# Performance work log

Measured on AMD Instinct MI355X. Metric: run time of the kernel, lower is better.

## Reference

```python
import jax, jax.numpy as jnp
import numpy as np
import math

B, S, D, H, NF = 2, 2048, 1024, 16, 4
DH = D // H


def setup_inputs() -> dict:
    key = jax.random.key(0)
    ks = jax.random.split(key, 8)
    scale = 0.01 / math.sqrt(D)  # rough attenuated-kaiming scale for projections
    return {
        "x": jax.random.normal(ks[0], (B, S, D), dtype=jnp.float32),
        "weights": jax.random.uniform(ks[1], (1, NF), dtype=jnp.float32),
        "Wq": jax.random.normal(ks[2], (D, D), dtype=jnp.float32) * scale,
        "bq": jnp.zeros((D,), dtype=jnp.float32),
        "Wk": jax.random.normal(ks[3], (D, D), dtype=jnp.float32) * scale,
        "bk": jnp.zeros((D,), dtype=jnp.float32),
        "Wv": jax.random.normal(ks[4], (D, D), dtype=jnp.float32) * scale,
        "bv": jnp.zeros((D,), dtype=jnp.float32),
        "Wout": jax.random.normal(ks[5], (NF, D, D), dtype=jnp.float32) / math.sqrt(D),
        "bout": jnp.zeros((NF, D), dtype=jnp.float32),
    }


def reference(x, weights, Wq, bq, Wk, bk, Wv, bv, Wout, bout):
    # projections (torch Linear: x @ W.T + b)
    q = x @ Wq.T + bq  # [B,S,D]
    k = x @ Wk.T + bk
    v = x @ Wv.T + bv
    # split heads -> [B,H,S,DH]
    split = lambda t: t.reshape(B, S, H, DH).transpose(0, 2, 1, 3)
    q, k, v = split(q), split(k), split(v)
    # scores with causal additive mask of -10000 (as in get_attention_mask)
    scores = jnp.einsum("bhqd,bhkd->bhqk", q, k) / math.sqrt(DH)
    i = jnp.arange(S)
    causal = (i[None, :] <= i[:, None])  # [S,S] True where allowed
    mask = (1.0 - causal.astype(scores.dtype)) * -10000.0
    attn = jax.nn.softmax(scores + mask, axis=-1)
    # dropout is disabled (p=0.0)
    out = jnp.einsum("bhqk,bhkd->bhqd", attn, v)  # [B,H,S,DH]
    out = out.transpose(0, 2, 1, 3).reshape(B, S, D)
    # WeightedFunctions: per-function Linear(d,d) combined by weights[0]
    w0 = weights[0]  # [NF]
    Weff = jnp.einsum("f,fod->od", w0, Wout)  # [D,D]
    beff = w0 @ bout  # [D]
    return out @ Weff.T + beff
```

## Files before the change

### kernel.cpp

```cpp
#include <hip/hip_runtime.h>

typedef unsigned short u16;
typedef __bf16 bf16_t;
typedef bf16_t bf16x8 __attribute__((ext_vector_type(8)));
typedef bf16_t bf16x4 __attribute__((ext_vector_type(4)));
typedef float f32x4 __attribute__((ext_vector_type(4)));
typedef u16 u16x8 __attribute__((ext_vector_type(8)));
typedef u16 u16x4 __attribute__((ext_vector_type(4)));

#define DEV __device__ __forceinline__

DEV u16 f2bf(float f) {
  unsigned u = __float_as_uint(f);
  u += 0x7FFFu + ((u >> 16) & 1u);
  return (u16)(u >> 16);
}

DEV void async_ld16(const void* g, void* lds_wave_uniform) {
  __builtin_amdgcn_global_load_lds(
      (const __attribute__((address_space(1))) void*)g,
      (__attribute__((address_space(3))) void*)lds_wave_uniform, 16, 0, 0);
}

DEV int KF(int r) { return (r & 3) ^ ((r >> 2) & 1); }

__global__ __launch_bounds__(256) void prep_kernel(
    const float* __restrict__ x, const float* __restrict__ Wq,
    const float* __restrict__ Wk, const float* __restrict__ Wv,
    const float* __restrict__ w4, const float* __restrict__ Wout,
    const float* __restrict__ bout, u16* __restrict__ xbf,
    u16* __restrict__ wqkv, u16* __restrict__ Weff, float* __restrict__ beff) {
  constexpr int NX = 1048576;
  constexpr int NW = 262144;
  const int stride = gridDim.x * 256;
  for (int id = blockIdx.x * 256 + threadIdx.x; id < NX + 3 * NW + NW;
       id += stride) {
    if (id < NX) {
      const float4 v = ((const float4*)x)[id];
      u16x4 o;
      o[0] = f2bf(v.x); o[1] = f2bf(v.y); o[2] = f2bf(v.z); o[3] = f2bf(v.w);
      ((u16x4*)xbf)[id] = o;
    } else if (id < NX + 3 * NW) {
      const int wi = id - NX;
      const int which = wi >> 18, j = wi & (NW - 1);
      const float* src = which == 0 ? Wq : (which == 1 ? Wk : Wv);
      const float4 v = ((const float4*)src)[j];
      u16x4 o;
      o[0] = f2bf(v.x); o[1] = f2bf(v.y); o[2] = f2bf(v.z); o[3] = f2bf(v.w);
      ((u16x4*)wqkv)[wi] = o;
    } else {
      const int i = id - NX - 3 * NW;
      const float w0 = w4[0], w1 = w4[1], w2 = w4[2], w3 = w4[3];
      const float4* W = (const float4*)Wout;
      const float4 a = W[i], b1 = W[NW + i], b2 = W[2 * NW + i],
                   b3 = W[3 * NW + i];
      u16x4 o;
      o[0] = f2bf(w0 * a.x + w1 * b1.x + w2 * b2.x + w3 * b3.x);
      o[1] = f2bf(w0 * a.y + w1 * b1.y + w2 * b2.y + w3 * b3.y);
      o[2] = f2bf(w0 * a.z + w1 * b1.z + w2 * b2.z + w3 * b3.z);
      o[3] = f2bf(w0 * a.w + w1 * b1.w + w2 * b2.w + w3 * b3.w);
      ((u16x4*)Weff)[i] = o;
      if (i < 256) {
        const float4* B4 = (const float4*)bout;
        const float4 ba = B4[i], c1 = B4[256 + i], c2 = B4[512 + i],
                     c3 = B4[768 + i];
        float4 ob;
        ob.x = w0 * ba.x + w1 * c1.x + w2 * c2.x + w3 * c3.x;
        ob.y = w0 * ba.y + w1 * c1.y + w2 * c2.y + w3 * c3.y;
        ob.z = w0 * ba.z + w1 * c1.z + w2 * c2.z + w3 * c3.z;
        ob.w = w0 * ba.w + w1 * c1.w + w2 * c2.w + w3 * c3.w;
        ((float4*)beff)[i] = ob;
      }
    }
  }
}

#define GEMM_PIPELINE_LOOP(A_, B_, m0_, n0_, K_)                               \
  int rA[2], oA[2], dstc[2];                                                   \
  _Pragma("unroll") for (int j = 0; j < 2; ++j) {                              \
    const int c = (j * 4 + w) * 64 + lane;                                     \
    rA[j] = c >> 2;                                                            \
    oA[j] = ((c & 3) ^ KF(rA[j])) * 8;                                         \
    dstc[j] = (j * 4 + w) * 512;                                               \
  }                                                                            \
  auto stage = [&](int buf, int kt) {                                          \
    _Pragma("unroll") for (int j = 0; j < 2; ++j) {                            \
      async_ld16(A_ + (m0_ + rA[j]) * K_ + kt + oA[j],                         \
                 &LDS[buf * 4096 + dstc[j]]);                                  \
      async_ld16(B_ + (n0_ + rA[j]) * K_ + kt + oA[j],                         \
                 &LDS[12288 + buf * 4096 + dstc[j]]);                          \
    }                                                                          \
  };                                                                           \
  f32x4 acc[4][4] = {};                                                        \
  stage(0, 0);                                                                 \
  stage(1, 32);                                                                \
  const int nt = K_ / 32;                                                      \
  int cur = 0, stg = 2;                                                        \
  for (int t = 0; t < nt; ++t) {                                               \
    if (t == nt - 1)                                                           \
      asm volatile("s_waitcnt vmcnt(0)\ns_barrier" ::: "memory");              \
    else                                                                       \
      asm volatile("s_waitcnt vmcnt(4)\ns_barrier" ::: "memory");              \
    __builtin_amdgcn_sched_barrier(0);                                         \
    if (t + 2 < nt) stage(stg, (t + 2) * 32);                                  \
    bf16x8 af[4], bfr[4];                                                      \
    _Pragma("unroll") for (int i = 0; i < 4; ++i) {                            \
      const int ra = wr * 64 + i * 16 + l15;                                   \
      const int rb = wc * 64 + i * 16 + l15;                                   \
      af[i] = *(const bf16x8*)&LDS[cur * 4096 + ra * 32 + ((l4 ^ KF(ra)) * 8)];\
      bfr[i] = *(const bf16x8*)&LDS[12288 + cur * 4096 + rb * 32 +             \
                                    ((l4 ^ KF(rb)) * 8)];                      \
    }                                                                          \
    __builtin_amdgcn_s_setprio(1);                                             \
    _Pragma("unroll") for (int i = 0; i < 4; ++i)                              \
        _Pragma("unroll") for (int j = 0; j < 4; ++j)                          \
            acc[i][j] = __builtin_amdgcn_mfma_f32_16x16x32_bf16(               \
                af[i], bfr[j], acc[i][j], 0, 0, 0);                            \
    __builtin_amdgcn_s_setprio(0);                                             \
    cur = cur == 2 ? 0 : cur + 1;                                              \
    stg = stg == 2 ? 0 : stg + 1;                                              \
  }

__global__ __launch_bounds__(256) void gemm_bt_kernel(
    const u16* __restrict__ A, const u16* __restrict__ Bw,
    const float* __restrict__ bias, float* __restrict__ C, int M, int N, int K) {
  __shared__ u16 LDS[24576];
  const int tid = threadIdx.x;
  const int w = tid >> 6, lane = tid & 63;
  const int l15 = lane & 15, l4 = lane >> 4;
  const int wr = w >> 1, wc = w & 1;
  const long m0 = (long)blockIdx.y * 128, n0 = (long)blockIdx.x * 128;

  GEMM_PIPELINE_LOOP(A, Bw, m0, n0, K)

#pragma unroll
  for (int i = 0; i < 4; ++i) {
    const long row0 = m0 + wr * 64 + i * 16 + l4 * 4;
#pragma unroll
    for (int j = 0; j < 4; ++j) {
      const long col = n0 + wc * 64 + j * 16 + l15;
      const float bb = bias[col];
#pragma unroll
      for (int r = 0; r < 4; ++r)
        C[(row0 + r) * N + col] = acc[i][j][r] + bb;
    }
  }
}

__global__ __launch_bounds__(512) void gemm_qkv_kernel(
    const u16* __restrict__ A, const u16* __restrict__ Bw,
    const float* __restrict__ bq, const float* __restrict__ bk,
    const float* __restrict__ bv, u16* __restrict__ qo, u16* __restrict__ ko,
    u16* __restrict__ vt) {
  constexpr int K = 1024;
  __shared__ u16 LDS[49152];
  const int tid = threadIdx.x;
  const int w = tid >> 6, lane = tid & 63;
  const int l15 = lane & 15, l4 = lane >> 4;
  const int wr = w >> 2, wc = w & 3;
  const long m0 = (long)blockIdx.y * 256, n0 = (long)blockIdx.x * 256;
  const int seg = blockIdx.x >> 2;
  const float* bias = seg == 0 ? bq : (seg == 1 ? bk : bv);
  const float scale = seg == 0 ? 0.18033688011112042f : 1.0f;

  int rA[2], oA[2], dstc[2];
#pragma unroll
  for (int j = 0; j < 2; ++j) {
    const int c = (j * 8 + w) * 64 + lane;
    rA[j] = c >> 2;
    oA[j] = ((c & 3) ^ KF(rA[j])) * 8;
    dstc[j] = (j * 8 + w) * 512;
  }
  auto stage = [&](int buf, int kt) {
#pragma unroll
    for (int j = 0; j < 2; ++j) {
      async_ld16(A + (m0 + rA[j]) * K + kt + oA[j],
                 &LDS[buf * 8192 + dstc[j]]);
      async_ld16(Bw + (n0 + rA[j]) * K + kt + oA[j],
                 &LDS[24576 + buf * 8192 + dstc[j]]);
    }
  };

  f32x4 acc[8][4] = {};
  stage(0, 0);
  stage(1, 32);
  const int nt = K / 32;
  int cur = 0, stg = 2;
  for (int t = 0; t < nt; ++t) {
    if (t == nt - 1)
      asm volatile("s_waitcnt vmcnt(0)\ns_barrier" ::: "memory");
    else
      asm volatile("s_waitcnt vmcnt(4)\ns_barrier" ::: "memory");
    __builtin_amdgcn_sched_barrier(0);
    if (t + 2 < nt) stage(stg, (t + 2) * 32);
    bf16x8 af[8], bfr[4];
#pragma unroll
    for (int i = 0; i < 8; ++i) {
      const int ra = wr * 128 + i * 16 + l15;
      af[i] = *(const bf16x8*)&LDS[cur * 8192 + ra * 32 + ((l4 ^ KF(ra)) * 8)];
    }
#pragma unroll
    for (int j = 0; j < 4; ++j) {
      const int rb = wc * 64 + j * 16 + l15;
      bfr[j] = *(const bf16x8*)&LDS[24576 + cur * 8192 + rb * 32 +
                                    ((l4 ^ KF(rb)) * 8)];
    }
    __builtin_amdgcn_s_setprio(1);
#pragma unroll
    for (int i = 0; i < 8; ++i)
#pragma unroll
      for (int j = 0; j < 4; ++j)
        acc[i][j] = __builtin_amdgcn_mfma_f32_16x16x32_bf16(af[i], bfr[j],
                                                            acc[i][j], 0, 0, 0);
    __builtin_amdgcn_s_setprio(0);
    cur = cur == 2 ? 0 : cur + 1;
    stg = stg == 2 ? 0 : stg + 1;
  }

  __syncthreads();
  const long ccol0 = n0 - (long)seg * 1024;
  if (seg < 2) {
    u16* outp = seg == 0 ? qo : ko;
#pragma unroll
    for (int h = 0; h < 2; ++h) {
      if ((wc >> 1) == h) {
#pragma unroll
        for (int i = 0; i < 8; ++i)
#pragma unroll
          for (int j = 0; j < 4; ++j) {
            const int colb = (wc & 1) * 64 + j * 16 + l15;
            const float bb = bias[ccol0 + h * 128 + colb];
#pragma unroll
            for (int r = 0; r < 4; ++r) {
              const int row = wr * 128 + i * 16 + l4 * 4 + r;
              LDS[row * 128 + (colb ^ ((row & 15) << 3))] =
                  f2bf((acc[i][j][r] + bb) * scale);
            }
          }
      }
      __syncthreads();
#pragma unroll
      for (int p = 0; p < 8; ++p) {
        const int cid = p * 512 + tid;
        const int row = cid >> 4, c = cid & 15;
        const u16x8 vch =
            *(const u16x8*)&LDS[row * 128 + ((c ^ (row & 15)) * 8)];
        *(u16x8*)&outp[(m0 + row) * 1024 + ccol0 + h * 128 + c * 8] = vch;
      }
      __syncthreads();
    }
  } else {
    const int b = (int)(m0 >> 11);
    const int s0 = (int)(m0 & 2047);
#pragma unroll
    for (int h = 0; h < 2; ++h) {
      if ((wc >> 1) == h) {
#pragma unroll
        for (int i = 0; i < 8; ++i)
#pragma unroll
          for (int j = 0; j < 4; ++j) {
            const int colb = (wc & 1) * 64 + j * 16 + l15;
            const float bb = bias[ccol0 + h * 128 + colb];
#pragma unroll
            for (int r = 0; r < 4; ++r) {
              const int row = wr * 128 + i * 16 + l4 * 4 + r;
              LDS[colb * 256 + (row ^ ((colb & 15) << 3))] =
                  f2bf(acc[i][j][r] + bb);
            }
          }
      }
      __syncthreads();
#pragma unroll
      for (int p = 0; p < 8; ++p) {
        const int cid = p * 512 + tid;
        const int c = cid >> 5, r0 = (cid & 31) * 8;
        const u16x8 vch = *(const u16x8*)&LDS[c * 256 + (r0 ^ ((c & 15) << 3))];
        const int gcol = (int)ccol0 + h * 128 + c;
        const int hh = gcol >> 6, d = gcol & 63;
        *(u16x8*)&vt[(size_t)((b * 16 + hh) * 64 + d) * 2048 + s0 + r0] = vch;
      }
      __syncthreads();
    }
  }
}

__global__ __launch_bounds__(512) void flash_kernel(
    const u16* __restrict__ Q, const u16* __restrict__ Kg,
    const u16* __restrict__ Vt, u16* __restrict__ O,
    u16* __restrict__ accP, float* __restrict__ mP, float* __restrict__ lP) {
  constexpr int S = 2048, D = 1024, DH = 64;
  __shared__ u16 Ks[3][4096];
  __shared__ u16 Vs[3][4096];
  __shared__ u16 Ps[8][2048];
  const int tid = threadIdx.x;
  const int w = tid >> 6, lane = tid & 63;
  const int l15 = lane & 15, l4 = lane >> 4;
  const int bh = blockIdx.x, b = bh >> 4, h = bh & 15;
  const int xb = blockIdx.y;
  const int p = xb >> 1, seg = xb & 1;
  const int p1len = seg ? 0 : 4 * p + 4;
  const int kvoff = seg ? (14 - 4 * p) : 0;
  const int TA = seg ? (7 - p) : p;
  const int TB = 7 - p;
  const int qbA_keep = TA * 256 + w * 32;

  const u16* Kbh = Kg + (size_t)b * S * D + h * DH;
  const u16* Vbh = Vt + (size_t)bh * DH * S;

  const int srow = tid >> 3;
  const int scol = ((tid & 7) ^ (srow & 7)) * 8;
  const int sw = l15 & 7;

  bf16x8 qf[2][2], qfB[2][2];
#pragma unroll
  for (int c = 0; c < 2; ++c) {
    const u16* qp =
        Q + (size_t)(b * S + qbA_keep + c * 16 + l15) * D + h * DH + l4 * 8;
    qf[c][0] = *(const bf16x8*)qp;
    qf[c][1] = *(const bf16x8*)(qp + 32);
    qfB[c][0] = qf[c][0];
    qfB[c][1] = qf[c][1];
  }
  if (!seg) {
    const int qbB = TB * 256 + w * 32;
#pragma unroll
    for (int c = 0; c < 2; ++c) {
      const u16* qp =
          Q + (size_t)(b * S + qbB + c * 16 + l15) * D + h * DH + l4 * 8;
      qfB[c][0] = *(const bf16x8*)qp;
      qfB[c][1] = *(const bf16x8*)(qp + 32);
    }
  }

  f32x4 acc_o[2][4] = {};
  float m_run[2] = {-3e38f, -3e38f};
  float l_run[2] = {0.f, 0.f};

  int qb = qbA_keep;
  int qt64w = TA * 4 + (w >> 1);

  auto kv_of = [&](int j) { return (j < p1len) ? j : (j - p1len + kvoff); };
  auto stage = [&](int kv, int buf) {
    async_ld16(Kbh + (size_t)(kv * 64 + srow) * D + scol, &Ks[buf][w * 512]);
    async_ld16(Vbh + (size_t)srow * S + kv * 64 + scol, &Vs[buf][w * 512]);
  };

  stage(kv_of(0), 0);
  stage(kv_of(1), 1);

  constexpr int NST = 18;
  for (int j = 0; j < NST; ++j) {
    if (j == NST - 1)
      asm volatile("s_waitcnt vmcnt(0)\ns_barrier" ::: "memory");
    else
      asm volatile("s_waitcnt vmcnt(2)\ns_barrier" ::: "memory");
    __builtin_amdgcn_sched_barrier(0);
    if (j + 2 < NST) stage(kv_of(j + 2), (j + 2) % 3);

    if (seg == 0 && j == p1len) {
      float lt[2], lq[2][4];
#pragma unroll
      for (int c = 0; c < 2; ++c) {
        float t = l_run[c];
        t += __shfl_xor(t, 16);
        t += __shfl_xor(t, 32);
        lt[c] = t;
#pragma unroll
        for (int r = 0; r < 4; ++r) lq[c][r] = __shfl(lt[c], l4 * 4 + r, 64);
      }
#pragma unroll
      for (int c = 0; c < 2; ++c)
#pragma unroll
        for (int db = 0; db < 4; ++db)
#pragma unroll
          for (int r = 0; r < 4; ++r) {
            const int row = c * 16 + l4 * 4 + r;
            const int col = db * 16 + l15;
            Ps[w][row * 64 + (col ^ ((row & 7) << 3))] =
                f2bf(acc_o[c][db][r] / lq[c][r]);
          }
      asm volatile("s_waitcnt lgkmcnt(0)" ::: "memory");
#pragma unroll
      for (int j4 = 0; j4 < 4; ++j4) {
        const int cid = j4 * 64 + lane;
        const int row = cid >> 3, c8 = cid & 7;
        const u16x8 vch =
            *(const u16x8*)&Ps[w][row * 64 + ((c8 ^ (row & 7)) * 8)];
        *(u16x8*)&O[(size_t)(b * S + qbA_keep + row) * D + h * DH + c8 * 8] =
            vch;
      }
#pragma unroll
      for (int c = 0; c < 2; ++c) {
        qf[c][0] = qfB[c][0];
        qf[c][1] = qfB[c][1];
        m_run[c] = -3e38f;
        l_run[c] = 0.f;
#pragma unroll
        for (int db = 0; db < 4; ++db) acc_o[c][db] = f32x4{0.f, 0.f, 0.f, 0.f};
      }
      qb = TB * 256 + w * 32;
      qt64w = TB * 4 + (w >> 1);
    }

    const int it = kv_of(j);
    const int buf = j % 3;
    if (it <= qt64w) {
      f32x4 accs[2][4] = {};
      __builtin_amdgcn_s_setprio(1);
#pragma unroll
      for (int cb = 0; cb < 4; ++cb) {
        const int row = cb * 16 + l15;
        const bf16x8 kf0 = *(const bf16x8*)&Ks[buf][row * 64 + ((l4 ^ sw) * 8)];
        const bf16x8 kf1 =
            *(const bf16x8*)&Ks[buf][row * 64 + (((l4 + 4) ^ sw) * 8)];
#pragma unroll
        for (int c = 0; c < 2; ++c) {
          accs[c][cb] = __builtin_amdgcn_mfma_f32_16x16x32_bf16(
              kf0, qf[c][0], accs[c][cb], 0, 0, 0);
          accs[c][cb] = __builtin_amdgcn_mfma_f32_16x16x32_bf16(
              kf1, qf[c][1], accs[c][cb], 0, 0, 0);
        }
      }
      __builtin_amdgcn_s_setprio(0);
      bf16x8 vf0[4], vf1[4];
#pragma unroll
      for (int db = 0; db < 4; ++db) {
        const int row = db * 16 + l15;
        vf0[db] = *(const bf16x8*)&Vs[buf][row * 64 + ((l4 ^ sw) * 8)];
        vf1[db] = *(const bf16x8*)&Vs[buf][row * 64 + (((l4 + 4) ^ sw) * 8)];
      }
      float mx[2] = {-3e38f, -3e38f};
      if (it == qt64w) {
#pragma unroll
        for (int c = 0; c < 2; ++c)
#pragma unroll
          for (int cb = 0; cb < 4; ++cb)
#pragma unroll
            for (int r = 0; r < 4; ++r) {
              float s_ = accs[c][cb][r];
              if (it * 64 + cb * 16 + l4 * 4 + r > qb + c * 16 + l15)
                s_ = -3e38f;
              accs[c][cb][r] = s_;
              mx[c] = fmaxf(mx[c], s_);
            }
      } else {
#pragma unroll
        for (int c = 0; c < 2; ++c)
#pragma unroll
          for (int cb = 0; cb < 4; ++cb)
#pragma unroll
            for (int r = 0; r < 4; ++r) mx[c] = fmaxf(mx[c], accs[c][cb][r]);
      }
      if (!__all(fmaxf(mx[0] - m_run[0], mx[1] - m_run[1]) <= 8.0f)) {
#pragma unroll
        for (int c = 0; c < 2; ++c) {
          float m = mx[c];
          m = fmaxf(m, __shfl_xor(m, 16));
          m = fmaxf(m, __shfl_xor(m, 32));
          const float mn = fmaxf(m_run[c], m);
          const float corr = __builtin_amdgcn_exp2f(m_run[c] - mn);
          m_run[c] = mn;
          float cq[4];
#pragma unroll
          for (int r = 0; r < 4; ++r) cq[r] = __shfl(corr, l4 * 4 + r, 64);
#pragma unroll
          for (int db = 0; db < 4; ++db)
#pragma unroll
            for (int r = 0; r < 4; ++r) acc_o[c][db][r] *= cq[r];
          l_run[c] *= corr;
        }
      }
#pragma unroll
      for (int c = 0; c < 2; ++c) {
        float rs = 0.f;
#pragma unroll
        for (int cb = 0; cb < 4; ++cb)
#pragma unroll
          for (int r = 0; r < 4; ++r) {
            const float pv = __builtin_amdgcn_exp2f(accs[c][cb][r] - m_run[c]);
            accs[c][cb][r] = pv;
            rs += pv;
          }
        l_run[c] += rs;
      }
#pragma unroll
      for (int c = 0; c < 2; ++c)
#pragma unroll
        for (int cb = 0; cb < 4; ++cb) {
          bf16x4 pk = {(bf16_t)accs[c][cb][0], (bf16_t)accs[c][cb][1],
                       (bf16_t)accs[c][cb][2], (bf16_t)accs[c][cb][3]};
          const int chunk = (2 * cb + (l4 >> 1)) ^ sw;
          *(bf16x4*)&Ps[w][(c * 16 + l15) * 64 + chunk * 8 + (l4 & 1) * 4] = pk;
        }
      asm volatile("s_waitcnt lgkmcnt(0)" ::: "memory");
      bf16x8 pa[2][2];
#pragma unroll
      for (int c = 0; c < 2; ++c)
#pragma unroll
        for (int mf = 0; mf < 2; ++mf) {
          const int chunk = (mf * 4 + l4) ^ sw;
          pa[c][mf] =
              *(const bf16x8*)&Ps[w][(c * 16 + l15) * 64 + chunk * 8];
        }
      __builtin_amdgcn_s_setprio(1);
#pragma unroll
      for (int db = 0; db < 4; ++db) {
#pragma unroll
        for (int c = 0; c < 2; ++c) {
          acc_o[c][db] = __builtin_amdgcn_mfma_f32_16x16x32_bf16(
              pa[c][0], vf0[db], acc_o[c][db], 0, 0, 0);
          acc_o[c][db] = __builtin_amdgcn_mfma_f32_16x16x32_bf16(
              pa[c][1], vf1[db], acc_o[c][db], 0, 0, 0);
        }
      }
      __builtin_amdgcn_s_setprio(0);
    }
  }

  float lt[2];
#pragma unroll
  for (int c = 0; c < 2; ++c) {
    float t = l_run[c];
    t += __shfl_xor(t, 16);
    t += __shfl_xor(t, 32);
    lt[c] = t;
  }
#pragma unroll
  for (int c = 0; c < 2; ++c)
#pragma unroll
    for (int db = 0; db < 4; ++db)
#pragma unroll
      for (int r = 0; r < 4; ++r) {
        const int row = c * 16 + l4 * 4 + r;
        const int col = db * 16 + l15;
        Ps[w][row * 64 + (col ^ ((row & 7) << 3))] = f2bf(acc_o[c][db][r]);
      }
  asm volatile("s_waitcnt lgkmcnt(0)" ::: "memory");
  const size_t base =
      (size_t)seg * 32768 + (size_t)bh * 1024 + (TB * 256 + w * 32 - 1024);
#pragma unroll
  for (int j4 = 0; j4 < 4; ++j4) {
    const int cid = j4 * 64 + lane;
    const int row = cid >> 3, c8 = cid & 7;
    const u16x8 vch = *(const u16x8*)&Ps[w][row * 64 + ((c8 ^ (row & 7)) * 8)];
    *(u16x8*)&accP[(base + row) * 64 + c8 * 8] = vch;
  }
  if (l4 == 0) {
#pragma unroll
    for (int c = 0; c < 2; ++c) {
      mP[base + c * 16 + l15] = m_run[c];
      lP[base + c * 16 + l15] = lt[c];
    }
  }
}

__global__ __launch_bounds__(256) void combine_kernel(
    const u16* __restrict__ accP, const float* __restrict__ mP,
    const float* __restrict__ lP, u16* __restrict__ O) {
  const int id = blockIdx.x * 256 + threadIdx.x;
  const int row = id >> 3;
  const int c0 = (id & 7) * 8;
  const float m0 = mP[row], m1 = mP[32768 + row];
  const float l0 = lP[row], l1 = lP[32768 + row];
  const float M = fmaxf(m0, m1);
  const float e0 = __builtin_amdgcn_exp2f(m0 - M);
  const float e1 = __builtin_amdgcn_exp2f(m1 - M);
  const float inv = 1.f / (l0 * e0 + l1 * e1);
  const bf16_t* aP = (const bf16_t*)accP;
  const bf16x8 a0 = *(const bf16x8*)&aP[(size_t)row * 64 + c0];
  const bf16x8 a1 = *(const bf16x8*)&aP[(size_t)(32768 + row) * 64 + c0];
  const int bh = row >> 10, s = 1024 + (row & 1023);
  const int b = bh >> 4, h = bh & 15;
  bf16_t* out = (bf16_t*)O + (size_t)(b * 2048 + s) * 1024 + h * 64 + c0;
  bf16x8 o;
#pragma unroll
  for (int j = 0; j < 8; ++j)
    o[j] = (bf16_t)(((float)a0[j] * e0 + (float)a1[j] * e1) * inv);
  *(bf16x8*)out = o;
}

extern "C" void kernel_launch(void* const* d_in, const int* in_sizes, int n_in,
                              void* d_out, int out_size, void* d_ws, size_t ws_size,
                              hipStream_t stream) {
  (void)in_sizes; (void)n_in; (void)out_size;
  const float* x   = (const float*)d_in[0];
  const float* wts = (const float*)d_in[1];
  const float* Wq  = (const float*)d_in[2];
  const float* bq  = (const float*)d_in[3];
  const float* Wk  = (const float*)d_in[4];
  const float* bk  = (const float*)d_in[5];
  const float* Wv  = (const float*)d_in[6];
  const float* bv  = (const float*)d_in[7];
  const float* Wo  = (const float*)d_in[8];
  const float* bo  = (const float*)d_in[9];
  float* out = (float*)d_out;

  if (ws_size < 58724352) return;

  char* ws = (char*)d_ws;
  u16* xbf  = (u16*)(ws + 0);
  u16* qbf  = (u16*)(ws + 8388608);
  u16* kbf  = (u16*)(ws + 16777216);
  u16* vt   = (u16*)(ws + 33554432);
  u16* attn = (u16*)(ws + 41943040);
  u16* wqkv = (u16*)(ws + 50331648);
  u16* wob  = (u16*)(ws + 56623104);
  float* beff = (float*)(ws + 58720256);

  u16* accP = xbf;
  float* mP = (float*)(ws + 50331648);
  float* lP = mP + 65536;

  prep_kernel<<<2048, 256, 0, stream>>>(x, Wq, Wk, Wv, wts, Wo, bo,
                                        xbf, wqkv, wob, beff);
  gemm_qkv_kernel<<<dim3(12, 16), 512, 0, stream>>>(xbf, wqkv, bq, bk, bv,
                                                    qbf, kbf, vt);
  flash_kernel<<<dim3(32, 8), 512, 0, stream>>>(qbf, kbf, vt, attn,
                                                accP, mP, lP);
  combine_kernel<<<1024, 256, 0, stream>>>(accP, mP, lP, attn);
  gemm_bt_kernel<<<dim3(8, 32), 256, 0, stream>>>(
      attn, wob, beff, out, 4096, 1024, 1024);
}
```

Before: 107.7 us.

## Interleave LDS reads, async global loads and MFMAs in four phases per k-tile

Restructures the QKV projection GEMM main loop so each k-tile is split into four phases. Each phase loads two A fragments, issues one slice of the next-next tile's async global-to-LDS loads, then runs eight MFMAs, with barriers between phases. The aim is to spread memory issue across the MFMA work instead of bunching it at the start of the tile, and to keep fewer A fragments live in registers at once. In exchange it adds several extra s_barriers per tile, which may stall waves, and the vmcnt accounting changes.

```diff
diff --git a/kernel.cpp b/kernel.cpp
--- a/kernel.cpp
+++ b/kernel.cpp
@@ -171,50 +171,65 @@
     oA[j] = ((c & 3) ^ KF(rA[j])) * 8;
     dstc[j] = (j * 8 + w) * 512;
   }
-  auto stage = [&](int buf, int kt) {
-#pragma unroll
-    for (int j = 0; j < 2; ++j) {
-      async_ld16(A + (m0 + rA[j]) * K + kt + oA[j],
-                 &LDS[buf * 8192 + dstc[j]]);
-      async_ld16(Bw + (n0 + rA[j]) * K + kt + oA[j],
-                 &LDS[24576 + buf * 8192 + dstc[j]]);
-    }
+  auto stageA = [&](int slab, int kt, int j) {
+    async_ld16(A + (m0 + rA[j]) * K + kt + oA[j], &LDS[slab * 8192 + dstc[j]]);
   };
+  auto stageB = [&](int slab, int kt, int j) {
+    async_ld16(Bw + (n0 + rA[j]) * K + kt + oA[j],
+               &LDS[24576 + slab * 8192 + dstc[j]]);
+  };
 
   f32x4 acc[8][4] = {};
-  stage(0, 0);
-  stage(1, 32);
+  stageA(0, 0, 0); stageA(0, 0, 1); stageB(0, 0, 0); stageB(0, 0, 1);
+  stageA(1, 32, 0); stageA(1, 32, 1); stageB(1, 32, 0); stageB(1, 32, 1);
+  asm volatile("s_waitcnt vmcnt(4)\ns_barrier" ::: "memory");
+
   const int nt = K / 32;
-  int cur = 0, stg = 2;
   for (int t = 0; t < nt; ++t) {
-    if (t == nt - 1)
+    const int s = t % 3;
+    const int s2 = (t + 2) % 3;
+    const int kt2 = (t + 2) * 32;
+    const bool st = (t + 2) < nt;
+    bf16x8 bfr[4];
+#pragma unroll
+    for (int ph = 0; ph < 4; ++ph) {
+      if (ph == 0) {
+#pragma unroll
+        for (int j = 0; j < 4; ++j) {
+          const int rb = wc * 64 + j * 16 + l15;
+          bfr[j] = *(const bf16x8*)&LDS[24576 + s * 8192 + rb * 32 +
+                                        ((l4 ^ KF(rb)) * 8)];
+        }
+      }
+      const int ra0 = wr * 128 + (2 * ph) * 16 + l15;
+      const int ra1 = wr * 128 + (2 * ph + 1) * 16 + l15;
+      const bf16x8 af0 =
+          *(const bf16x8*)&LDS[s * 8192 + ra0 * 32 + ((l4 ^ KF(ra0)) * 8)];
+      const bf16x8 af1 =
+          *(const bf16x8*)&LDS[s * 8192 + ra1 * 32 + ((l4 ^ KF(ra1)) * 8)];
+      if (st) {
+        if (ph == 0) stageA(s2, kt2, 0);
+        else if (ph == 1) stageA(s2, kt2, 1);
+        else if (ph == 2) stageB(s2, kt2, 0);
+        else stageB(s2, kt2, 1);
+      }
+      asm volatile("s_barrier" ::: "memory");
+      asm volatile("s_waitcnt lgkmcnt(0)" ::: "memory");
+      __builtin_amdgcn_s_setprio(1);
+#pragma unroll
+      for (int j = 0; j < 4; ++j) {
+        acc[2 * ph][j] = __builtin_amdgcn_mfma_f32_16x16x32_bf16(
+            af0, bfr[j], acc[2 * ph][j], 0, 0, 0);
+        acc[2 * ph + 1][j] = __builtin_amdgcn_mfma_f32_16x16x32_bf16(
+            af1, bfr[j], acc[2 * ph + 1][j], 0, 0, 0);
+      }
+      __builtin_amdgcn_s_setprio(0);
+      if (ph < 3) asm volatile("s_barrier" ::: "memory");
+    }
+    if (t >= nt - 3)
       asm volatile("s_waitcnt vmcnt(0)\ns_barrier" ::: "memory");
     else
       asm volatile("s_waitcnt vmcnt(4)\ns_barrier" ::: "memory");
-    __builtin_amdgcn_sched_barrier(0);
-    if (t + 2 < nt) stage(stg, (t + 2) * 32);
-    bf16x8 af[8], bfr[4];
-#pragma unroll
-    for (int i = 0; i < 8; ++i) {
-      const int ra = wr * 128 + i * 16 + l15;
-      af[i] = *(const bf16x8*)&LDS[cur * 8192 + ra * 32 + ((l4 ^ KF(ra)) * 8)];
-    }
-#pragma unroll
-    for (int j = 0; j < 4; ++j) {
-      const int rb = wc * 64 + j * 16 + l15;
-      bfr[j] = *(const bf16x8*)&LDS[24576 + cur * 8192 + rb * 32 +
-                                    ((l4 ^ KF(rb)) * 8)];
-    }
-    __builtin_amdgcn_s_setprio(1);
-#pragma unroll
-    for (int i = 0; i < 8; ++i)
-#pragma unroll
-      for (int j = 0; j < 4; ++j)
-        acc[i][j] = __builtin_amdgcn_mfma_f32_16x16x32_bf16(af[i], bfr[j],
-                                                            acc[i][j], 0, 0, 0);
-    __builtin_amdgcn_s_setprio(0);
-    cur = cur == 2 ? 0 : cur + 1;
-    stg = stg == 2 ? 0 : stg + 1;
   }
 
   __syncthreads();
```

Result: slower. 111.7 us (+3.8%).

## Restructure QKV GEMM to double-buffered BK=64 pipeline with interleaved staging

Applied to the files above, without the earlier changes.

The QKV projection GEMM moves from a triple-buffered K=32 pipeline to a double-buffered K=64 pipeline (128 KB LDS). Loads for the next tile are issued in four phases interleaved with the MFMA work, which cuts barrier count in half and changes the LDS swizzle to an 8-way XOR. The output GEMM also swaps its block index mapping so consecutive blocks walk along M instead of N, which changes L2 reuse of weight tiles. The cost is a full vmcnt(0) wait every iteration and higher LDS use.

```diff
diff --git a/kernel.cpp b/kernel.cpp
--- a/kernel.cpp
+++ b/kernel.cpp
@@ -129,7 +129,7 @@
   const int w = tid >> 6, lane = tid & 63;
   const int l15 = lane & 15, l4 = lane >> 4;
   const int wr = w >> 1, wc = w & 1;
-  const long m0 = (long)blockIdx.y * 128, n0 = (long)blockIdx.x * 128;
+  const long m0 = (long)blockIdx.x * 128, n0 = (long)blockIdx.y * 128;
 
   GEMM_PIPELINE_LOOP(A, Bw, m0, n0, K)
 
@@ -153,7 +153,7 @@
     const float* __restrict__ bv, u16* __restrict__ qo, u16* __restrict__ ko,
     u16* __restrict__ vt) {
   constexpr int K = 1024;
-  __shared__ u16 LDS[49152];
+  __shared__ u16 LDS[65536];
   const int tid = threadIdx.x;
   const int w = tid >> 6, lane = tid & 63;
   const int l15 = lane & 15, l4 = lane >> 4;
@@ -163,58 +163,66 @@
   const float* bias = seg == 0 ? bq : (seg == 1 ? bk : bv);
   const float scale = seg == 0 ? 0.18033688011112042f : 1.0f;
 
-  int rA[2], oA[2], dstc[2];
-#pragma unroll
-  for (int j = 0; j < 2; ++j) {
-    const int c = (j * 8 + w) * 64 + lane;
-    rA[j] = c >> 2;
-    oA[j] = ((c & 3) ^ KF(rA[j])) * 8;
-    dstc[j] = (j * 8 + w) * 512;
-  }
-  auto stage = [&](int buf, int kt) {
-#pragma unroll
-    for (int j = 0; j < 2; ++j) {
-      async_ld16(A + (m0 + rA[j]) * K + kt + oA[j],
-                 &LDS[buf * 8192 + dstc[j]]);
-      async_ld16(Bw + (n0 + rA[j]) * K + kt + oA[j],
-                 &LDS[24576 + buf * 8192 + dstc[j]]);
-    }
+  const int sr0 = tid >> 3;
+  const int soff = ((tid & 7) ^ ((tid >> 3) & 7)) * 8;
+  auto stage_half = [&](int k, int h) {
+    const int slot = k & 1;
+    const int base =
+        (h < 2 ? 0 : 32768) + slot * 16384 + (h & 1) * 8192;
+    const long row0 = (h < 2 ? m0 : n0) + (h & 1) * 128;
+    const u16* M = (h < 2) ? A : Bw;
+    const int kt = k * 64;
+    async_ld16(M + (row0 + sr0) * K + kt + soff, &LDS[base + w * 512]);
+    async_ld16(M + (row0 + 64 + sr0) * K + kt + soff,
+               &LDS[base + 4096 + w * 512]);
   };
 
   f32x4 acc[8][4] = {};
-  stage(0, 0);
-  stage(1, 32);
-  const int nt = K / 32;
-  int cur = 0, stg = 2;
-  for (int t = 0; t < nt; ++t) {
-    if (t == nt - 1)
-      asm volatile("s_waitcnt vmcnt(0)\ns_barrier" ::: "memory");
-    else
-      asm volatile("s_waitcnt vmcnt(4)\ns_barrier" ::: "memory");
-    __builtin_amdgcn_sched_barrier(0);
-    if (t + 2 < nt) stage(stg, (t + 2) * 32);
-    bf16x8 af[8], bfr[4];
-#pragma unroll
-    for (int i = 0; i < 8; ++i) {
-      const int ra = wr * 128 + i * 16 + l15;
-      af[i] = *(const bf16x8*)&LDS[cur * 8192 + ra * 32 + ((l4 ^ KF(ra)) * 8)];
-    }
+#pragma unroll
+  for (int h = 0; h < 4; ++h) stage_half(0, h);
+
+  for (int t = 0; t < 16; ++t) {
+    asm volatile("s_waitcnt vmcnt(0)\ns_barrier" ::: "memory");
+    const int slot = t & 1;
+    const int abase = slot * 16384;
+    const int bbase = 32768 + slot * 16384;
+    const bool st = (t + 1) < 16;
+    bf16x8 bfr[4][2];
 #pragma unroll
     for (int j = 0; j < 4; ++j) {
       const int rb = wc * 64 + j * 16 + l15;
-      bfr[j] = *(const bf16x8*)&LDS[24576 + cur * 8192 + rb * 32 +
-                                    ((l4 ^ KF(rb)) * 8)];
-    }
-    __builtin_amdgcn_s_setprio(1);
-#pragma unroll
-    for (int i = 0; i < 8; ++i)
-#pragma unroll
-      for (int j = 0; j < 4; ++j)
-        acc[i][j] = __builtin_amdgcn_mfma_f32_16x16x32_bf16(af[i], bfr[j],
-                                                            acc[i][j], 0, 0, 0);
-    __builtin_amdgcn_s_setprio(0);
-    cur = cur == 2 ? 0 : cur + 1;
-    stg = stg == 2 ? 0 : stg + 1;
+#pragma unroll
+      for (int ks = 0; ks < 2; ++ks)
+        bfr[j][ks] = *(const bf16x8*)&LDS[bbase + rb * 64 +
+                                          (((ks * 4 + l4) ^ (rb & 7)) * 8)];
+    }
+#pragma unroll
+    for (int ph = 0; ph < 4; ++ph) {
+      if (st) stage_half(t + 1, ph);
+      const int ra0 = wr * 128 + (2 * ph) * 16 + l15;
+      const int ra1 = wr * 128 + (2 * ph + 1) * 16 + l15;
+      bf16x8 af0[2], af1[2];
+#pragma unroll
+      for (int ks = 0; ks < 2; ++ks) {
+        af0[ks] = *(const bf16x8*)&LDS[abase + ra0 * 64 +
+                                       (((ks * 4 + l4) ^ (ra0 & 7)) * 8)];
+        af1[ks] = *(const bf16x8*)&LDS[abase + ra1 * 64 +
+                                       (((ks * 4 + l4) ^ (ra1 & 7)) * 8)];
+      }
+      __builtin_amdgcn_s_setprio(1);
+#pragma unroll
+      for (int j = 0; j < 4; ++j) {
+        acc[2 * ph][j] = __builtin_amdgcn_mfma_f32_16x16x32_bf16(
+            af0[0], bfr[j][0], acc[2 * ph][j], 0, 0, 0);
+        acc[2 * ph][j] = __builtin_amdgcn_mfma_f32_16x16x32_bf16(
+            af0[1], bfr[j][1], acc[2 * ph][j], 0, 0, 0);
+        acc[2 * ph + 1][j] = __builtin_amdgcn_mfma_f32_16x16x32_bf16(
+            af1[0], bfr[j][0], acc[2 * ph + 1][j], 0, 0, 0);
+        acc[2 * ph + 1][j] = __builtin_amdgcn_mfma_f32_16x16x32_bf16(
+            af1[1], bfr[j][1], acc[2 * ph + 1][j], 0, 0, 0);
+      }
+      __builtin_amdgcn_s_setprio(0);
+    }
   }
 
   __syncthreads();
@@ -618,6 +626,6 @@
   flash_kernel<<<dim3(32, 8), 512, 0, stream>>>(qbf, kbf, vt, attn,
                                                 accP, mP, lP);
   combine_kernel<<<1024, 256, 0, stream>>>(accP, mP, lP, attn);
-  gemm_bt_kernel<<<dim3(8, 32), 256, 0, stream>>>(
+  gemm_bt_kernel<<<dim3(32, 8), 256, 0, stream>>>(
       attn, wob, beff, out, 4096, 1024, 1024);
 }
```

Result: faster. 103.3 us, median of 2 (-4.1%).
